# Performance work log

Measured on AMD Instinct MI355X. Metric: run time of the kernel, lower is better.

## Reference

```python
import jax, jax.numpy as jnp
import numpy as np

# Config (matches init_kwargs)
N_PARTS = 4
N_DATASETS = 2
N_VOLUMES = 16
N_TRANSFORMS = 2
TEMP_FAC = 0.1
BS = N_PARTS * N_DATASETS * N_VOLUMES          # 128
N_TOTAL = BS * (N_TRANSFORMS + 1)              # 384 rows in reg_pred
D_FEAT = 131072
PD = N_PARTS * N_DATASETS                      # class period for denominator exclusion
EPS = 1e-6


def setup_inputs() -> dict:
    key = jax.random.key(0)
    reg_pred = jax.random.normal(key, (N_TOTAL, D_FEAT), dtype=jnp.float32)
    return {"reg_pred": reg_pred}


def reference(reg_pred) -> jnp.ndarray:
    # Cosine similarity with torch's eps clamp on each norm.
    norms = jnp.maximum(jnp.linalg.norm(reg_pred, axis=1, keepdims=True), EPS)
    xn = reg_pred / norms                                   # [N, D]
    sims = (xn @ xn.T) / TEMP_FAC                           # [N, N] full cos-sim matrix
    e = jnp.exp(sims)

    # Denominator for pos_index p excludes every column j with j % PD == p % PD
    # (dataset_similar=False, within_dataset=False). Precompute per-class column sums.
    jmod = jnp.arange(N_TOTAL) % PD                          # [N]
    class_sum = jax.ops.segment_sum(e.T, jmod, num_segments=PD).T  # [N, PD]
    row_sum = jnp.sum(e, axis=1)                             # [N]

    p = jnp.arange(BS)
    rem = p % PD
    i1 = p
    i2 = BS + p
    i3 = (p + PD) % N_TOTAL
    i4 = (BS + p + PD) % N_TOTAL
    i5 = 2 * BS + p
    i6 = (2 * BS + p + PD) % N_TOTAL

    def pair_loss(a, b):
        en = e[a, b]                                         # exp(cos(xi,xj)/t), [BS]
        den_a = row_sum[a] - class_sum[a, rem]               # sum exp over den indexes
        den_b = row_sum[b] - class_sum[b, rem]
        return jnp.sum(-jnp.log(en / (en + den_a)) - jnp.log(en / (en + den_b)))

    total = (pair_loss(i1, i2) + pair_loss(i3, i4) + pair_loss(i1, i3)
             + pair_loss(i2, i4) + pair_loss(i5, i6) + pair_loss(i2, i5)
             + pair_loss(i4, i6))
    return total / (N_TRANSFORMS * 3 * BS)
```

## Files before the change

### kernel.cpp

```cpp
#include <hip/hip_runtime.h>
#include <hip/hip_bf16.h>

#define N_TOTAL 384
#define BS 128
#define PD 8
#define D_FEAT 131072
#define EPS 1e-6f

#define NSTRIP 256
#define COLS_PER (D_FEAT / NSTRIP)
#define CHUNK 32
#define NCH (COLS_PER / CHUNK)
#define NSLOT 24

typedef __attribute__((ext_vector_type(4))) float f32x4;
typedef __attribute__((ext_vector_type(8))) __bf16 bf16x8;
typedef __attribute__((ext_vector_type(4))) __bf16 bf16x4;

typedef __attribute__((address_space(1))) const unsigned int gu32;
typedef __attribute__((address_space(3))) unsigned int lu32;

__device__ __forceinline__ void gload16(const void* g, void* l) {
    __builtin_amdgcn_global_load_lds((gu32*)g, (lu32*)l, 16, 0, 0);
}

static __device__ const int SAt[8][3] = {{0,0,0},{0,0,0},{1,1,1},{1,1,1},
                                         {2,2,4},{2,2,4},{3,3,5},{3,3,5}};
static __device__ const int SBt[8][3] = {{0,1,2},{3,4,5},{0,1,2},{3,4,5},
                                         {2,3,4},{4,5,5},{2,3,4},{4,5,5}};
static __device__ const int SRB2[NSLOT] = {0,0,0, 0,0,0, 1,1,1, 1,1,1,
                                           2,2,4, 2,2,4, 3,3,5, 3,3,5};
static __device__ const int SCB2[NSLOT] = {0,1,2, 3,4,5, 0,1,2, 3,4,5,
                                           2,3,4, 4,5,5, 2,3,4, 4,5,5};

__device__ __forceinline__ float gsym(const float* __restrict__ G, int i, int j) {
    return ((i >> 7) <= (j >> 7)) ? G[(size_t)i * N_TOTAL + j]
                                  : G[(size_t)j * N_TOTAL + i];
}

__global__ __launch_bounds__(512) void gram_fused_kernel(const float* __restrict__ X,
                                                         __bf16* __restrict__ P) {
    __shared__ char smf[2][N_TOTAL * 128];
    __shared__ char smb[2][N_TOTAL * 64];

    const int strip = blockIdx.x;
    const int tid  = threadIdx.x;
    const int wave = tid >> 6;
    const int lane = tid & 63;
    const int r16  = lane & 15;
    const int kg   = lane >> 4;

    const int A0 = SAt[wave][0] * 64, A2 = SAt[wave][2] * 64;
    const int B0 = SBt[wave][0] * 64, B1 = SBt[wave][1] * 64, B2 = SBt[wave][2] * 64;

    const char* src0 = (const char*)(X + (size_t)(tid >> 3) * D_FEAT
                                       + (size_t)strip * COLS_PER) + (tid & 7) * 16;

    f32x4 acc0[4][4], acc1[4][4], acc2[4][4];
#pragma unroll
    for (int m = 0; m < 4; m++)
#pragma unroll
        for (int n = 0; n < 4; n++) {
            acc0[m][n] = (f32x4)(0.0f); acc1[m][n] = (f32x4)(0.0f); acc2[m][n] = (f32x4)(0.0f);
        }

#define STAGE(buf, t)                                                                     \
    _Pragma("unroll") for (int s = 0; s < 6; s++)                                         \
        gload16(src0 + (size_t)s * (64ull * D_FEAT * 4) + (size_t)(t) * 128,              \
                (char*)smf[buf] + s * 8192 + tid * 16);

#define SUBT(accX, Bb)                                                                    \
    do {                                                                                  \
        bf16x8 bf[4];                                                                     \
        _Pragma("unroll") for (int n = 0; n < 4; n++)                                     \
            bf[n] = *(const bf16x8*)(bptr + ((Bb) + n * 16 + r16) * 64 + kg * 16);        \
        _Pragma("unroll") for (int m = 0; m < 4; m++)                                     \
            _Pragma("unroll") for (int n = 0; n < 4; n++)                                 \
                accX[m][n] = __builtin_amdgcn_mfma_f32_16x16x32_bf16(af[m], bf[n],        \
                                                                     accX[m][n], 0, 0, 0);\
    } while (0)

    STAGE(0, 0);
    STAGE(1, 1);

    for (int t = 0; t < NCH; ++t) {
        const int b = t & 1;
        if (t < NCH - 1) asm volatile("s_waitcnt vmcnt(6)" ::: "memory");
        else             asm volatile("s_waitcnt vmcnt(0)" ::: "memory");
        __builtin_amdgcn_sched_barrier(0);
        __builtin_amdgcn_s_barrier();
        __builtin_amdgcn_sched_barrier(0);

        {
            const char* fb = smf[b];
            char*       bb = smb[b];
#pragma unroll
            for (int s = 0; s < 6; s++) {
                const f32x4 v = *(const f32x4*)(fb + (size_t)s * 8192 + tid * 16);
                bf16x4 o;
                o[0] = (__bf16)v[0]; o[1] = (__bf16)v[1];
                o[2] = (__bf16)v[2]; o[3] = (__bf16)v[3];
                *(bf16x4*)(bb + (size_t)s * 4096 + tid * 8) = o;
            }
        }

        asm volatile("s_waitcnt lgkmcnt(0)" ::: "memory");
        __builtin_amdgcn_sched_barrier(0);
        __builtin_amdgcn_s_barrier();
        __builtin_amdgcn_sched_barrier(0);
        if (t + 2 < NCH) STAGE(b, t + 2);

        const char* bptr = smb[b];
        bf16x8 af[4];
#pragma unroll
        for (int m = 0; m < 4; m++)
            af[m] = *(const bf16x8*)(bptr + (A0 + m * 16 + r16) * 64 + kg * 16);
        SUBT(acc0, B0);
        SUBT(acc1, B1);
#pragma unroll
        for (int m = 0; m < 4; m++)
            af[m] = *(const bf16x8*)(bptr + (A2 + m * 16 + r16) * 64 + kg * 16);
        SUBT(acc2, B2);
    }
#undef STAGE
#undef SUBT

    const int crow = (lane >> 4) * 4;
    const int ccol = lane & 15;
#define STOREP(accX, s)                                                                   \
    do {                                                                                  \
        __bf16* base = P + ((size_t)strip * NSLOT + wave * 3 + (s)) * 4096;               \
        _Pragma("unroll") for (int m = 0; m < 4; m++)                                     \
            _Pragma("unroll") for (int n = 0; n < 4; n++) {                               \
                bf16x4 v;                                                                 \
                v[0] = (__bf16)accX[m][n][0]; v[1] = (__bf16)accX[m][n][1];               \
                v[2] = (__bf16)accX[m][n][2]; v[3] = (__bf16)accX[m][n][3];               \
                *(bf16x4*)(base + (n * 16 + ccol) * 64 + m * 16 + crow) = v;              \
            }                                                                             \
    } while (0)
    STOREP(acc0, 0);
    STOREP(acc1, 1);
    STOREP(acc2, 2);
#undef STOREP
}

__global__ __launch_bounds__(128) void reduce_kernel(const __bf16* __restrict__ P,
                                                     float* __restrict__ G) {
    const int gidx = blockIdx.x * 128 + threadIdx.x;
    const int slot = gidx >> 11;
    const int pe   = (gidx & 2047) * 2;

    const unsigned* p = (const unsigned*)(P + (size_t)slot * 4096 + pe);
    const size_t stride = (size_t)NSLOT * 4096 / 2;
    float s0 = 0.0f, s1 = 0.0f;
#pragma unroll 16
    for (int strip = 0; strip < NSTRIP; ++strip) {
        const unsigned u = p[stride * strip];
        s0 += __uint_as_float(u << 16);
        s1 += __uint_as_float(u & 0xffff0000u);
    }

    const int rb  = SRB2[slot] * 64;
    const int cb  = SCB2[slot] * 64;
    const int col = pe >> 6;
    const int row = pe & 63;
    G[(size_t)(rb + row)     * N_TOTAL + cb + col] = s0;
    G[(size_t)(rb + row + 1) * N_TOTAL + cb + col] = s1;
}

__global__ __launch_bounds__(128) void den_kernel(const float* __restrict__ G,
                                                  float* __restrict__ den) {
    const int i = blockIdx.x;
    __shared__ float sInv[N_TOTAL];
    for (int j = threadIdx.x; j < N_TOTAL; j += 128) {
        const float n = sqrtf(G[(size_t)j * N_TOTAL + j]);
        sInv[j] = 1.0f / fmaxf(n, EPS);
    }
    __syncthreads();

    const float mi  = sInv[i] * 10.0f;
    const int   myc = i & 7;
    float s = 0.0f;
    for (int j = threadIdx.x; j < N_TOTAL; j += 128) {
        if ((j & 7) != myc)
            s += expf(gsym(G, i, j) * mi * sInv[j]);
    }
#pragma unroll
    for (int off = 32; off > 0; off >>= 1) s += __shfl_down(s, off, 64);
    __shared__ float partial[2];
    if ((threadIdx.x & 63) == 0) partial[threadIdx.x >> 6] = s;
    __syncthreads();
    if (threadIdx.x == 0) den[i] = partial[0] + partial[1];
}

__global__ __launch_bounds__(256) void loss_kernel(const float* __restrict__ G,
                                                   const float* __restrict__ den,
                                                   float* __restrict__ out) {
    __shared__ float sInv[N_TOTAL];
    for (int j = threadIdx.x; j < N_TOTAL; j += 256) {
        const float n = sqrtf(G[(size_t)j * N_TOTAL + j]);
        sInv[j] = 1.0f / fmaxf(n, EPS);
    }
    __syncthreads();

    float s = 0.0f;
    for (int idx = threadIdx.x; idx < 7 * BS; idx += 256) {
        const int p   = idx & (BS - 1);
        const int set = idx >> 7;
        int a, b;
        switch (set) {
            case 0:  a = p;                        b = BS + p;                      break;
            case 1:  a = (p + PD) % N_TOTAL;       b = (BS + p + PD) % N_TOTAL;     break;
            case 2:  a = p;                        b = (p + PD) % N_TOTAL;          break;
            case 3:  a = BS + p;                   b = (BS + p + PD) % N_TOTAL;     break;
            case 4:  a = 2 * BS + p;               b = (2 * BS + p + PD) % N_TOTAL; break;
            case 5:  a = BS + p;                   b = 2 * BS + p;                  break;
            default: a = (BS + p + PD) % N_TOTAL;  b = (2 * BS + p + PD) % N_TOTAL; break;
        }
        const float en = expf(gsym(G, a, b) * sInv[a] * sInv[b] * 10.0f);
        s += log1pf(den[a] / en) + log1pf(den[b] / en);
    }
#pragma unroll
    for (int off = 32; off > 0; off >>= 1) s += __shfl_down(s, off, 64);
    __shared__ float partial[4];
    if ((threadIdx.x & 63) == 0) partial[threadIdx.x >> 6] = s;
    __syncthreads();
    if (threadIdx.x == 0)
        out[0] = (partial[0] + partial[1] + partial[2] + partial[3]) / 768.0f;
}

extern "C" void kernel_launch(void* const* d_in, const int* in_sizes, int n_in,
                              void* d_out, int out_size, void* d_ws, size_t ws_size,
                              hipStream_t stream) {
    (void)in_sizes; (void)n_in; (void)out_size; (void)ws_size;
    const float* X   = (const float*)d_in[0];
    float*       out = (float*)d_out;
    float*       G   = (float*)d_ws;
    float*       den = G + (size_t)N_TOTAL * N_TOTAL;
    __bf16*      P   = (__bf16*)((char*)d_ws + (1u << 20));

    gram_fused_kernel<<<NSTRIP, 512, 0, stream>>>(X, P);
    reduce_kernel<<<384, 128, 0, stream>>>(P, G);
    den_kernel<<<N_TOTAL, 128, 0, stream>>>(G, den);
    loss_kernel<<<1, 256, 0, stream>>>(G, den, out);
}
```

Measured before the change: 76.24 us.

## Double chunk width, single-buffer staging with XOR-swizzled bf16 LDS layout

Widens each K chunk from 32 to 64 columns and replaces the double-buffered fp32/bf16 LDS staging with a single buffer, so each chunk load is one larger sweep fully waited on before conversion. The bf16 tile rows become 128 bytes, and an XOR swizzle on the 16-byte group index is meant to avoid LDS bank conflicts on MFMA fragment reads. Each chunk now runs two k-steps of MFMAs, halving the barrier count. The trade-off is that the next chunk's global load is only overlapped with the MFMA phase instead of being prefetched two chunks ahead, and the vmcnt(0) wait exposes more load latency.

```diff
diff --git a/kernel.cpp b/kernel.cpp
--- a/kernel.cpp
+++ b/kernel.cpp
@@ -9,8 +9,9 @@
 
 #define NSTRIP 256
 #define COLS_PER (D_FEAT / NSTRIP)
-#define CHUNK 32
+#define CHUNK 64
 #define NCH (COLS_PER / CHUNK)
+#define NSWEEP 12
 #define NSLOT 24
 
 typedef __attribute__((ext_vector_type(4))) float f32x4;
@@ -38,10 +39,14 @@
                                   : G[(size_t)j * N_TOTAL + i];
 }
 
+__device__ __forceinline__ bf16x8 fragb(const char* smb, int row, int ks, int kg) {
+    return *(const bf16x8*)(smb + row * 128 + ((((ks << 2) | kg) ^ (row & 7)) << 4));
+}
+
 __global__ __launch_bounds__(512) void gram_fused_kernel(const float* __restrict__ X,
                                                          __bf16* __restrict__ P) {
-    __shared__ char smf[2][N_TOTAL * 128];
-    __shared__ char smb[2][N_TOTAL * 64];
+    __shared__ char smf[N_TOTAL * 256];
+    __shared__ char smb[N_TOTAL * 128];
 
     const int strip = blockIdx.x;
     const int tid  = threadIdx.x;
@@ -53,8 +58,12 @@
     const int A0 = SAt[wave][0] * 64, A2 = SAt[wave][2] * 64;
     const int B0 = SBt[wave][0] * 64, B1 = SBt[wave][1] * 64, B2 = SBt[wave][2] * 64;
 
-    const char* src0 = (const char*)(X + (size_t)(tid >> 3) * D_FEAT
-                                       + (size_t)strip * COLS_PER) + (tid & 7) * 16;
+    const char* src0 = (const char*)X + (size_t)(tid >> 4) * (D_FEAT * 4)
+                     + (size_t)strip * (COLS_PER * 4) + (tid & 15) * 16;
+
+    const int cr   = tid >> 4;
+    const int g16  = tid & 15;
+    const int wswz = ((((g16 >> 1) ^ (cr & 7)) << 4) | ((g16 & 1) << 3));
 
     f32x4 acc0[4][4], acc1[4][4], acc2[4][4];
 #pragma unroll
@@ -64,63 +73,56 @@
             acc0[m][n] = (f32x4)(0.0f); acc1[m][n] = (f32x4)(0.0f); acc2[m][n] = (f32x4)(0.0f);
         }
 
-#define STAGE(buf, t)                                                                     \
-    _Pragma("unroll") for (int s = 0; s < 6; s++)                                         \
-        gload16(src0 + (size_t)s * (64ull * D_FEAT * 4) + (size_t)(t) * 128,              \
-                (char*)smf[buf] + s * 8192 + tid * 16);
-
-#define SUBT(accX, Bb)                                                                    \
+#define STAGE(t)                                                                          \
+    _Pragma("unroll") for (int s = 0; s < NSWEEP; s++)                                    \
+        gload16(src0 + (size_t)s * (32ull * D_FEAT * 4) + (size_t)(t) * 256,              \
+                smf + s * 8192 + tid * 16);
+
+#define SUBT(accX, Bb, ks)                                                                \
     do {                                                                                  \
         bf16x8 bf[4];                                                                     \
         _Pragma("unroll") for (int n = 0; n < 4; n++)                                     \
-            bf[n] = *(const bf16x8*)(bptr + ((Bb) + n * 16 + r16) * 64 + kg * 16);        \
+            bf[n] = fragb(smb, (Bb) + n * 16 + r16, ks, kg);                              \
         _Pragma("unroll") for (int m = 0; m < 4; m++)                                     \
             _Pragma("unroll") for (int n = 0; n < 4; n++)                                 \
                 accX[m][n] = __builtin_amdgcn_mfma_f32_16x16x32_bf16(af[m], bf[n],        \
                                                                      accX[m][n], 0, 0, 0);\
     } while (0)
 
-    STAGE(0, 0);
-    STAGE(1, 1);
+    STAGE(0);
 
     for (int t = 0; t < NCH; ++t) {
-        const int b = t & 1;
-        if (t < NCH - 1) asm volatile("s_waitcnt vmcnt(6)" ::: "memory");
-        else             asm volatile("s_waitcnt vmcnt(0)" ::: "memory");
+        asm volatile("s_waitcnt vmcnt(0)" ::: "memory");
         __builtin_amdgcn_sched_barrier(0);
         __builtin_amdgcn_s_barrier();
         __builtin_amdgcn_sched_barrier(0);
 
-        {
-            const char* fb = smf[b];
-            char*       bb = smb[b];
-#pragma unroll
-            for (int s = 0; s < 6; s++) {
-                const f32x4 v = *(const f32x4*)(fb + (size_t)s * 8192 + tid * 16);
-                bf16x4 o;
-                o[0] = (__bf16)v[0]; o[1] = (__bf16)v[1];
-                o[2] = (__bf16)v[2]; o[3] = (__bf16)v[3];
-                *(bf16x4*)(bb + (size_t)s * 4096 + tid * 8) = o;
-            }
+#pragma unroll
+        for (int s = 0; s < NSWEEP; s++) {
+            const f32x4 v = *(const f32x4*)(smf + s * 8192 + tid * 16);
+            bf16x4 o;
+            o[0] = (__bf16)v[0]; o[1] = (__bf16)v[1];
+            o[2] = (__bf16)v[2]; o[3] = (__bf16)v[3];
+            *(bf16x4*)(smb + (s * 32 + cr) * 128 + wswz) = o;
         }
 
         asm volatile("s_waitcnt lgkmcnt(0)" ::: "memory");
         __builtin_amdgcn_sched_barrier(0);
         __builtin_amdgcn_s_barrier();
         __builtin_amdgcn_sched_barrier(0);
-        if (t + 2 < NCH) STAGE(b, t + 2);
-
-        const char* bptr = smb[b];
-        bf16x8 af[4];
-#pragma unroll
-        for (int m = 0; m < 4; m++)
-            af[m] = *(const bf16x8*)(bptr + (A0 + m * 16 + r16) * 64 + kg * 16);
-        SUBT(acc0, B0);
-        SUBT(acc1, B1);
-#pragma unroll
-        for (int m = 0; m < 4; m++)
-            af[m] = *(const bf16x8*)(bptr + (A2 + m * 16 + r16) * 64 + kg * 16);
-        SUBT(acc2, B2);
+        if (t + 1 < NCH) STAGE(t + 1);
+
+#pragma unroll
+        for (int ks = 0; ks < 2; ++ks) {
+            bf16x8 af[4];
+#pragma unroll
+            for (int m = 0; m < 4; m++) af[m] = fragb(smb, A0 + m * 16 + r16, ks, kg);
+            SUBT(acc0, B0, ks);
+            SUBT(acc1, B1, ks);
+#pragma unroll
+            for (int m = 0; m < 4; m++) af[m] = fragb(smb, A2 + m * 16 + r16, ks, kg);
+            SUBT(acc2, B2, ks);
+        }
     }
 #undef STAGE
 #undef SUBT
```

Result: faster. 71.41 us (-6.3%).
